# Kernel tuning notes

Measured on AMD Instinct MI355X. Metric: run time of the kernel, lower is better.

The kernel has to match this reference:

```python
import jax, jax.numpy as jnp
import numpy as np

B, S, D = 4, 2048, 1024
H, DK, DV = 16, 64, 64
FF = 4096
EPS = 1e-6


def _ln(x, g, b):
    mu = jnp.mean(x, axis=-1, keepdims=True)
    var = jnp.mean((x - mu) ** 2, axis=-1, keepdims=True)
    return (x - mu) * jax.lax.rsqrt(var + EPS) * g + b


def setup_inputs() -> dict:
    key = jax.random.key(0)
    ks = jax.random.split(key, 12)
    sd = 0.02
    return {
        "src": jax.random.normal(ks[0], (B, S, D), jnp.float32),
        "attn_mask": jnp.zeros((B, S, S), jnp.bool_),
        "Wq": jax.random.normal(ks[1], (D, H * DK), jnp.float32) * sd,
        "bq": jnp.zeros((H * DK,), jnp.float32),
        "Wk": jax.random.normal(ks[2], (D, H * DK), jnp.float32) * sd,
        "bk": jnp.zeros((H * DK,), jnp.float32),
        "Wv": jax.random.normal(ks[3], (D, H * DV), jnp.float32) * sd,
        "bv": jnp.zeros((H * DV,), jnp.float32),
        "Wo": jax.random.normal(ks[4], (D, D), jnp.float32) * sd,
        "bo": jnp.zeros((D,), jnp.float32),
        "ln1_g": jnp.ones((D,), jnp.float32),
        "ln1_b": jnp.zeros((D,), jnp.float32),
        "W1": jax.random.normal(ks[5], (D, FF), jnp.float32) * sd,
        "b1": jnp.zeros((FF,), jnp.float32),
        "W2": jax.random.normal(ks[6], (FF, D), jnp.float32) * sd,
        "b2": jnp.zeros((D,), jnp.float32),
        "ln2_g": jnp.ones((D,), jnp.float32),
        "ln2_b": jnp.zeros((D,), jnp.float32),
    }


def reference(src, attn_mask, Wq, bq, Wk, bk, Wv, bv, Wo, bo,
              ln1_g, ln1_b, W1, b1, W2, b2, ln2_g, ln2_b):
    # QKV projections, split heads: [B,S,H*dk] -> [B,H,S,dk]
    q = (src @ Wq + bq).reshape(B, S, H, DK).transpose(0, 2, 1, 3)
    k = (src @ Wk + bk).reshape(B, S, H, DK).transpose(0, 2, 1, 3)
    v = (src @ Wv + bv).reshape(B, S, H, DV).transpose(0, 2, 1, 3)

    scale = 1.0 / (DK ** 0.5)
    scores = jnp.einsum("bhqd,bhkd->bhqk", q, k) * scale
    scores = jnp.where(attn_mask[:, None, :, :], -1e9, scores)
    attn = jax.nn.softmax(scores, axis=-1)  # dropout = identity (eval)
    ctx = jnp.einsum("bhqk,bhkd->bhqd", attn, v)
    ctx = ctx.transpose(0, 2, 1, 3).reshape(B, S, D)

    att_out = ctx @ Wo + bo  # dropout = identity (eval)
    x = _ln(src + att_out, ln1_g, ln1_b)

    h = jax.nn.relu(x @ W1 + b1)  # dropout = identity (eval)
    ffn_out = h @ W2 + b2
    return _ln(ffn_out + x, ln2_g, ln2_b)
```

## Files before the change

kernel.cpp:

```cpp
#include <hip/hip_runtime.h>
#include <stdint.h>

#define BB 4
#define SS 2048
#define DMODEL 1024
#define NH 16
#define FF 4096
#define MROWS (BB*SS)

typedef __bf16 bf16x8 __attribute__((ext_vector_type(8)));
typedef __bf16 bf16x2t __attribute__((ext_vector_type(2)));
typedef float f32x4 __attribute__((ext_vector_type(4)));
typedef float f32x16 __attribute__((ext_vector_type(16)));
typedef unsigned uintx4 __attribute__((ext_vector_type(4)));

__device__ __forceinline__ unsigned short f2b(float f) {
  unsigned u = __float_as_uint(f);
  unsigned r = (u + 0x7FFFu + ((u >> 16) & 1u)) >> 16;
  return (unsigned short)r;
}
__device__ __forceinline__ float b2f(unsigned short u) {
  return __uint_as_float((unsigned)u << 16);
}

__device__ __forceinline__ unsigned pack2bf(float a, float b) {
  bf16x2t v = {(__bf16)a, (__bf16)b};
  return __builtin_bit_cast(unsigned, v);
}

__device__ __forceinline__ void pls32(unsigned& x, unsigned& y) {
#if defined(__has_builtin) && __has_builtin(__builtin_amdgcn_permlane32_swap)
  auto r = __builtin_amdgcn_permlane32_swap(x, y, 0, 0);
  x = (unsigned)r[0];
  y = (unsigned)r[1];
#else
  const unsigned sx = (unsigned)__shfl_xor((int)x, 32, 64);
  const unsigned sy = (unsigned)__shfl_xor((int)y, 32, 64);
  const bool hi = ((threadIdx.x >> 5) & 1) != 0;
  const unsigned nx = hi ? sy : x;
  const unsigned ny = hi ? y : sx;
  x = nx; y = ny;
#endif
}

__device__ __forceinline__ void gload_lds16(const void* g, void* l) {
  __builtin_amdgcn_global_load_lds(
      (const __attribute__((address_space(1))) void*)g,
      (__attribute__((address_space(3))) void*)l, 16, 0, 0);
}

__device__ __forceinline__ bf16x8 lds_frag(const unsigned short* base, int row, int k) {
  unsigned off = (unsigned)((row * 128 + k * 2) ^ ((row & 7) << 4));
  return *reinterpret_cast<const bf16x8*>(reinterpret_cast<const char*>(base) + off);
}

__device__ __forceinline__ bf16x8 frag_rot(const unsigned short* base, int row, int kElem) {
  const int cb = kElem * 2;
  const unsigned off = (unsigned)(row * 128 + ((((cb >> 4) + row) & 7) << 4) + (cb & 15));
  return *reinterpret_cast<const bf16x8*>(reinterpret_cast<const char*>(base) + off);
}

__global__ __launch_bounds__(256) void f32_to_bf16_k(const float* __restrict__ in,
                                                     unsigned short* __restrict__ out, int n8) {
  const int i = blockIdx.x * 256 + threadIdx.x;
  if (i >= n8) return;
  const float4* p = reinterpret_cast<const float4*>(in) + (size_t)i * 2;
  const float4 a = p[0], c = p[1];
  uint4 o;
  o.x = (unsigned)f2b(a.x) | ((unsigned)f2b(a.y) << 16);
  o.y = (unsigned)f2b(a.z) | ((unsigned)f2b(a.w) << 16);
  o.z = (unsigned)f2b(c.x) | ((unsigned)f2b(c.y) << 16);
  o.w = (unsigned)f2b(c.z) | ((unsigned)f2b(c.w) << 16);
  reinterpret_cast<uint4*>(out)[i] = o;
}

__global__ __launch_bounds__(256) void transpose_convert4_k(
    const float* __restrict__ i0, const float* __restrict__ i1,
    const float* __restrict__ i2, const float* __restrict__ i3,
    unsigned short* __restrict__ o0, unsigned short* __restrict__ o1,
    unsigned short* __restrict__ o2, unsigned short* __restrict__ o3) {
  __shared__ float tile[32][33];
  const int z = blockIdx.z;
  const float* in = (z == 0) ? i0 : (z == 1) ? i1 : (z == 2) ? i2 : i3;
  unsigned short* out = (z == 0) ? o0 : (z == 1) ? o1 : (z == 2) ? o2 : o3;
  const int c0 = blockIdx.x * 32, r0 = blockIdx.y * 32;
  const int tx = threadIdx.x, ty = threadIdx.y;
  #pragma unroll
  for (int i = 0; i < 4; ++i)
    tile[ty + i * 8][tx] = in[(size_t)(r0 + ty + i * 8) * 1024 + c0 + tx];
  __syncthreads();
  #pragma unroll
  for (int i = 0; i < 4; ++i)
    out[(size_t)(c0 + ty + i * 8) * 1024 + r0 + tx] = f2b(tile[tx][ty + i * 8]);
}

__global__ __launch_bounds__(256) void transpose_convert_k(const float* __restrict__ in,
                                                           unsigned short* __restrict__ out,
                                                           int R, int C) {
  __shared__ float tile[32][33];
  const int c0 = blockIdx.x * 32, r0 = blockIdx.y * 32;
  const int tx = threadIdx.x, ty = threadIdx.y;
  #pragma unroll
  for (int i = 0; i < 4; ++i)
    tile[ty + i * 8][tx] = in[(size_t)(r0 + ty + i * 8) * C + c0 + tx];
  __syncthreads();
  #pragma unroll
  for (int i = 0; i < 4; ++i)
    out[(size_t)(c0 + ty + i * 8) * R + r0 + tx] = f2b(tile[tx][ty + i * 8]);
}

__global__ __launch_bounds__(256) void v_transpose_k(const unsigned short* __restrict__ Vb,
                                                     unsigned short* __restrict__ Vt) {
  __shared__ unsigned short tile[32][33];
  const int bh = blockIdx.z, b = bh >> 4, h = bh & 15;
  const int s0 = blockIdx.x * 32, d0 = blockIdx.y * 32;
  const int tx = threadIdx.x, ty = threadIdx.y;
  #pragma unroll
  for (int i = 0; i < 4; ++i)
    tile[ty + i * 8][tx] = Vb[(size_t)(b * SS + s0 + ty + i * 8) * DMODEL + h * 64 + d0 + tx];
  __syncthreads();
  #pragma unroll
  for (int i = 0; i < 4; ++i)
    Vt[(size_t)(bh * 64 + d0 + ty + i * 8) * SS + s0 + tx] = tile[tx][ty + i * 8];
}

__global__ __launch_bounds__(256) void mask_pack_k(const unsigned char* __restrict__ mask,
                                                   unsigned long long* __restrict__ mbits, int total) {
  const int idx = blockIdx.x * 256 + threadIdx.x;
  if (idx >= total) return;
  const uint4* p = reinterpret_cast<const uint4*>(mask) + (size_t)idx * 4;
  unsigned long long bits = 0ull;
  #pragma unroll
  for (int q = 0; q < 4; ++q) {
    uint4 v = p[q];
    unsigned wds[4] = {v.x, v.y, v.z, v.w};
    #pragma unroll
    for (int j = 0; j < 4; ++j)
      #pragma unroll
      for (int by = 0; by < 4; ++by)
        if ((wds[j] >> (by * 8)) & 0xFFu) bits |= 1ull << (q * 16 + j * 4 + by);
  }
  mbits[idx] = bits;
}

#define CQ 0.18033688011112042f
template <int EPI>
__global__ __launch_bounds__(256, 3) void gemm2_k(const unsigned short* __restrict__ A,
                                                  const unsigned short* __restrict__ Bt,
                                                  const float* __restrict__ bias_a,
                                                  const float* __restrict__ bias_b,
                                                  const float* __restrict__ bias_c,
                                                  void* __restrict__ Cout, int N, int K) {
  __shared__ __align__(16) unsigned short As[2][128 * 64];
  __shared__ __align__(16) unsigned short Bs[2][128 * 64];
  const int t = threadIdx.x;
  const int lane = t & 63, w = t >> 6;
  const int wr = w >> 1, wc = w & 1;
  const int lr = lane & 15, lg = lane >> 4;

  const int nwg = gridDim.x;
  const int q8 = nwg >> 3;
  const int wg = (blockIdx.x & 7) * q8 + (blockIdx.x >> 3);
  const int sid = wg >> 6, within = wg & 63;
  const int smb = sid & 7, snb = sid >> 3;
  const int mb = smb * 8 + (within & 7);
  const int nb = snb * 8 + (within >> 3);
  const int m0 = mb * 128, n0 = nb * 128;

  const int srow = t >> 3;
  const unsigned cxor = (unsigned)(((t & 7) * 16) ^ (((t >> 3) & 7) << 4));
  const char* Asrc = reinterpret_cast<const char*>(A) + ((size_t)(m0 + srow) * K) * 2 + cxor;
  const char* Bsrc = reinterpret_cast<const char*>(Bt) + ((size_t)(n0 + srow) * K) * 2 + cxor;
  const size_t rstep = (size_t)32 * K * 2;
  char* AsB[2] = {reinterpret_cast<char*>(As[0]) + w * 1024, reinterpret_cast<char*>(As[1]) + w * 1024};
  char* BsB[2] = {reinterpret_cast<char*>(Bs[0]) + w * 1024, reinterpret_cast<char*>(Bs[1]) + w * 1024};

  auto stage = [&](int buf, int kt) {
    const char* ak = Asrc + (size_t)kt * 128;
    const char* bk = Bsrc + (size_t)kt * 128;
    #pragma unroll
    for (int c = 0; c < 4; ++c) {
      gload_lds16(ak + c * rstep, AsB[buf] + c * 4096);
      gload_lds16(bk + c * rstep, BsB[buf] + c * 4096);
    }
  };

  f32x4 acc[4][4] = {};
  const int nt = K >> 6;

  stage(0, 0);
  stage(1, 1);
  asm volatile("s_waitcnt vmcnt(8)" ::: "memory");
  __builtin_amdgcn_s_barrier();

  int cur = 0;
  for (int kt = 0; kt < nt; ++kt) {
    bf16x8 af[2][4], bfr[2][4];
    #pragma unroll
    for (int kk = 0; kk < 2; ++kk) {
      #pragma unroll
      for (int m = 0; m < 4; ++m)
        af[kk][m] = lds_frag(As[cur], wr * 64 + m * 16 + lr, kk * 32 + lg * 8);
      #pragma unroll
      for (int n = 0; n < 4; ++n)
        bfr[kk][n] = lds_frag(Bs[cur], wc * 64 + n * 16 + lr, kk * 32 + lg * 8);
    }
    __builtin_amdgcn_s_setprio(1);
    #pragma unroll
    for (int m = 0; m < 4; ++m)
      #pragma unroll
      for (int n = 0; n < 4; ++n)
        acc[m][n] = __builtin_amdgcn_mfma_f32_16x16x32_bf16(af[0][m], bfr[0][n], acc[m][n], 0, 0, 0);
    __builtin_amdgcn_s_setprio(0);

    asm volatile("s_waitcnt lgkmcnt(0)" ::: "memory");
    __builtin_amdgcn_s_barrier();
    if (kt + 2 < nt) {
      stage(cur, kt + 2);
      asm volatile("s_waitcnt vmcnt(8)" ::: "memory");
    } else {
      asm volatile("s_waitcnt vmcnt(0)" ::: "memory");
    }
    __builtin_amdgcn_s_barrier();

    __builtin_amdgcn_s_setprio(1);
    #pragma unroll
    for (int m = 0; m < 4; ++m)
      #pragma unroll
      for (int n = 0; n < 4; ++n)
        acc[m][n] = __builtin_amdgcn_mfma_f32_16x16x32_bf16(af[1][m], bfr[1][n], acc[m][n], 0, 0, 0);
    __builtin_amdgcn_s_setprio(0);
    cur ^= 1;
  }

  const int ccol0 = wc * 64;
  if constexpr (EPI == 3) {
    const int g3 = n0 >> 10;
    const float* bias = (g3 == 0) ? bias_a : (g3 == 1) ? bias_b : bias_c;
    const float scl = (g3 == 0) ? CQ : 1.0f;
    unsigned short* Og = reinterpret_cast<unsigned short*>(Cout) + (size_t)g3 * MROWS * DMODEL;
    const int ncol0 = (n0 & 1023) + ccol0;
    float bv[4];
    #pragma unroll
    for (int n = 0; n < 4; ++n) bv[n] = bias[ncol0 + n * 16 + lr];
    #pragma unroll
    for (int m = 0; m < 4; ++m)
      #pragma unroll
      for (int n = 0; n < 4; ++n)
        #pragma unroll
        for (int i = 0; i < 4; ++i) {
          const float v = (acc[m][n][i] + bv[n]) * scl;
          const size_t row = (size_t)(m0 + wr * 64 + m * 16 + lg * 4 + i);
          Og[row * DMODEL + (ncol0 + n * 16 + lr)] = f2b(v);
        }
  } else {
    float bv[4];
    #pragma unroll
    for (int n = 0; n < 4; ++n) bv[n] = bias_a[n0 + ccol0 + n * 16 + lr];
    #pragma unroll
    for (int m = 0; m < 4; ++m)
      #pragma unroll
      for (int n = 0; n < 4; ++n)
        #pragma unroll
        for (int i = 0; i < 4; ++i) {
          float v = acc[m][n][i] + bv[n];
          if (EPI == 1) v = fmaxf(v, 0.0f);
          const size_t row = (size_t)(m0 + wr * 64 + m * 16 + lg * 4 + i);
          const size_t col = (size_t)(n0 + ccol0 + n * 16 + lr);
          reinterpret_cast<unsigned short*>(Cout)[row * N + col] = f2b(v);
        }
  }
}

__global__ __launch_bounds__(256) void attn8_k(const unsigned short* __restrict__ Qb,
                                               const unsigned short* __restrict__ Kb,
                                               const unsigned short* __restrict__ Vt,
                                               const unsigned long long* __restrict__ mbits,
                                               unsigned short* __restrict__ ctx) {
  __shared__ __align__(16) unsigned short smem[16384];
  unsigned short* KsC = smem;
  unsigned short* KsN = smem + 4096;
  unsigned short* VsC = smem + 8192;
  unsigned short* VsN = smem + 12288;

  const int t = threadIdx.x;
  const int lane = t & 63, w = t >> 6;
  const int lo = lane & 31, hi = lane >> 5;

  const int flat = blockIdx.x;
  const int bid = (flat & 7) * 128 + (flat >> 3);
  const int bh = bid >> 4, qb = bid & 15;
  const int b = bh >> 4, h = bh & 15;
  const int q0 = qb * 128 + w * 32;

  bf16x8 qf[4];
  {
    const unsigned short* qp = Qb + (size_t)(b * SS + q0 + lo) * DMODEL + h * 64 + hi * 8;
    #pragma unroll
    for (int ds = 0; ds < 4; ++ds) qf[ds] = *reinterpret_cast<const bf16x8*>(qp + ds * 16);
  }

  const uintx4 onesw = {0x3F803F80u, 0x3F803F80u, 0x3F803F80u, 0x3F803F80u};
  const bf16x8 ones = __builtin_bit_cast(bf16x8, onesw);

  f32x16 ao0 = {}, ao1 = {}, dacc = {};

  const int srow = t >> 3;
  const int gsw = ((t & 7) - srow) & 7;
  const char* Ksrc = reinterpret_cast<const char*>(Kb) +
                     ((size_t)(b * SS + srow) * DMODEL + h * 64 + gsw * 8) * 2;
  const char* Vsrc = reinterpret_cast<const char*>(Vt) +
                     ((size_t)(bh * 64 + srow) * SS + gsw * 8) * 2;
  const unsigned wdo = (unsigned)(w * 1024);

  auto stage = [&](int kv, unsigned short* Kbuf, unsigned short* Vbuf) {
    const char* ks0 = Ksrc + (size_t)kv * (64 * DMODEL * 2);
    const char* vs0 = Vsrc + (size_t)kv * 128;
    char* kd = reinterpret_cast<char*>(Kbuf) + wdo;
    char* vd = reinterpret_cast<char*>(Vbuf) + wdo;
    gload_lds16(ks0, kd);
    gload_lds16(ks0 + (size_t)32 * DMODEL * 2, kd + 4096);
    gload_lds16(vs0, vd);
    gload_lds16(vs0 + (size_t)32 * SS * 2, vd + 4096);
  };

  const unsigned long long* mrow = mbits + (size_t)(b * SS + q0 + lo) * (SS / 64);

  stage(0, KsC, VsC);
  asm volatile("s_waitcnt vmcnt(0)" ::: "memory");
  __syncthreads();

  for (int kv = 0; kv < SS / 64; ++kv) {
    if (kv + 1 < SS / 64) stage(kv + 1, KsN, VsN);

    const unsigned long long mb = mrow[kv];

    f32x16 st0 = {}, st1 = {};
    __builtin_amdgcn_s_setprio(1);
    #pragma unroll
    for (int ds = 0; ds < 4; ++ds) {
      const int kcol = ds * 16 + hi * 8;
      const bf16x8 k0 = frag_rot(KsC, lo, kcol);
      const bf16x8 k1 = frag_rot(KsC, 32 + lo, kcol);
      st0 = __builtin_amdgcn_mfma_f32_32x32x16_bf16(k0, qf[ds], st0, 0, 0, 0);
      st1 = __builtin_amdgcn_mfma_f32_32x32x16_bf16(k1, qf[ds], st1, 0, 0, 0);
    }
    __builtin_amdgcn_s_setprio(0);

    if (__any(mb != 0ull)) {
      #pragma unroll
      for (int r = 0; r < 16; ++r) {
        const int k = (r & 3) + 8 * (r >> 2) + 4 * hi;
        if ((mb >> k) & 1ull) st0[r] = -20.0f;
        if ((mb >> (k + 32)) & 1ull) st1[r] = -20.0f;
      }
    }

    #pragma unroll
    for (int r = 0; r < 16; ++r) {
      st0[r] = exp2f(st0[r]);
      st1[r] = exp2f(st1[r]);
    }

    unsigned pw[16];
    #define PACK8(SV, KB)                                            \
      {                                                              \
        unsigned c0 = pack2bf(SV[0], SV[1]);                         \
        unsigned c1 = pack2bf(SV[2], SV[3]);                         \
        unsigned c2 = pack2bf(SV[4], SV[5]);                         \
        unsigned c3 = pack2bf(SV[6], SV[7]);                         \
        unsigned c4 = pack2bf(SV[8], SV[9]);                         \
        unsigned c5 = pack2bf(SV[10], SV[11]);                       \
        unsigned c6 = pack2bf(SV[12], SV[13]);                       \
        unsigned c7 = pack2bf(SV[14], SV[15]);                       \
        pls32(c0, c2); pls32(c1, c3); pls32(c4, c6); pls32(c5, c7);  \
        pw[(KB) + 0] = c0; pw[(KB) + 1] = c1;                        \
        pw[(KB) + 2] = c2; pw[(KB) + 3] = c3;                        \
        pw[(KB) + 4] = c4; pw[(KB) + 5] = c5;                        \
        pw[(KB) + 6] = c6; pw[(KB) + 7] = c7;                        \
      }
    PACK8(st0, 0)
    PACK8(st1, 8)
    #undef PACK8

    __builtin_amdgcn_s_setprio(1);
    #pragma unroll
    for (int ks = 0; ks < 4; ++ks) {
      const uintx4 pv = {pw[ks * 4 + 0], pw[ks * 4 + 1], pw[ks * 4 + 2], pw[ks * 4 + 3]};
      const bf16x8 pb = __builtin_bit_cast(bf16x8, pv);
      const int scol = ks * 16 + hi * 8;
      ao0 = __builtin_amdgcn_mfma_f32_32x32x16_bf16(frag_rot(VsC, lo, scol), pb, ao0, 0, 0, 0);
      ao1 = __builtin_amdgcn_mfma_f32_32x32x16_bf16(frag_rot(VsC, 32 + lo, scol), pb, ao1, 0, 0, 0);
      dacc = __builtin_amdgcn_mfma_f32_32x32x16_bf16(ones, pb, dacc, 0, 0, 0);
    }
    __builtin_amdgcn_s_setprio(0);

    asm volatile("s_waitcnt vmcnt(0)" ::: "memory");
    __syncthreads();
    unsigned short* tk = KsC; KsC = KsN; KsN = tk;
    unsigned short* tv = VsC; VsC = VsN; VsN = tv;
  }

  const float inv = 1.0f / dacc[0];
  unsigned short* Ob = smem + w * 2048;
  #pragma unroll
  for (int dt = 0; dt < 2; ++dt) {
    #pragma unroll
    for (int r = 0; r < 16; ++r) {
      const int d = dt * 32 + (r & 3) + 8 * (r >> 2) + 4 * hi;
      const float v = (dt ? ao1[r] : ao0[r]) * inv;
      const unsigned off = (unsigned)((lo * 128 + d * 2) ^ ((lo & 7) << 4));
      *reinterpret_cast<unsigned short*>(reinterpret_cast<char*>(Ob) + off) = f2b(v);
    }
  }
  __syncthreads();
  const int rr = lane >> 1, xh = (lane & 1) * 64;
  char* crow_g = reinterpret_cast<char*>(ctx) +
                 ((size_t)(b * SS + q0 + rr) * DMODEL + h * 64) * 2;
  #pragma unroll
  for (int c = 0; c < 4; ++c) {
    const unsigned off = (unsigned)((rr * 128 + xh + c * 16) ^ ((rr & 7) << 4));
    const uint4 vv = *reinterpret_cast<const uint4*>(reinterpret_cast<const char*>(Ob) + off);
    *reinterpret_cast<uint4*>(crow_g + xh + c * 16) = vv;
  }
}

__global__ __launch_bounds__(256) void ln1_k(const unsigned short* __restrict__ a,
                                             const float* __restrict__ res,
                                             const float* __restrict__ g,
                                             const float* __restrict__ be,
                                             unsigned short* __restrict__ ob) {
  const int row = blockIdx.x, t = threadIdx.x;
  const ushort4 av = reinterpret_cast<const ushort4*>(a + (size_t)row * DMODEL)[t];
  const float4 r = reinterpret_cast<const float4*>(res + (size_t)row * DMODEL)[t];
  float v0 = b2f(av.x) + r.x, v1 = b2f(av.y) + r.y;
  float v2 = b2f(av.z) + r.z, v3 = b2f(av.w) + r.w;
  float s = v0 + v1 + v2 + v3;
  float ss = v0 * v0 + v1 * v1 + v2 * v2 + v3 * v3;
  #pragma unroll
  for (int off = 1; off < 64; off <<= 1) {
    s += __shfl_xor(s, off, 64);
    ss += __shfl_xor(ss, off, 64);
  }
  __shared__ float red[8];
  const int wv = t >> 6;
  if ((t & 63) == 0) { red[wv] = s; red[4 + wv] = ss; }
  __syncthreads();
  s = red[0] + red[1] + red[2] + red[3];
  ss = red[4] + red[5] + red[6] + red[7];
  const float mu = s * (1.0f / DMODEL);
  const float rs = rsqrtf(ss * (1.0f / DMODEL) - mu * mu + 1e-6f);
  const float4 gg = reinterpret_cast<const float4*>(g)[t];
  const float4 bb = reinterpret_cast<const float4*>(be)[t];
  ushort4 u;
  u.x = f2b((v0 - mu) * rs * gg.x + bb.x);
  u.y = f2b((v1 - mu) * rs * gg.y + bb.y);
  u.z = f2b((v2 - mu) * rs * gg.z + bb.z);
  u.w = f2b((v3 - mu) * rs * gg.w + bb.w);
  reinterpret_cast<ushort4*>(ob + (size_t)row * DMODEL)[t] = u;
}

__global__ __launch_bounds__(256) void ln2_k(const unsigned short* __restrict__ a,
                                             const unsigned short* __restrict__ res,
                                             const float* __restrict__ g,
                                             const float* __restrict__ be,
                                             float* __restrict__ of) {
  const int row = blockIdx.x, t = threadIdx.x;
  const ushort4 av = reinterpret_cast<const ushort4*>(a + (size_t)row * DMODEL)[t];
  const ushort4 rv = reinterpret_cast<const ushort4*>(res + (size_t)row * DMODEL)[t];
  float v0 = b2f(av.x) + b2f(rv.x), v1 = b2f(av.y) + b2f(rv.y);
  float v2 = b2f(av.z) + b2f(rv.z), v3 = b2f(av.w) + b2f(rv.w);
  float s = v0 + v1 + v2 + v3;
  float ss = v0 * v0 + v1 * v1 + v2 * v2 + v3 * v3;
  #pragma unroll
  for (int off = 1; off < 64; off <<= 1) {
    s += __shfl_xor(s, off, 64);
    ss += __shfl_xor(ss, off, 64);
  }
  __shared__ float red[8];
  const int wv = t >> 6;
  if ((t & 63) == 0) { red[wv] = s; red[4 + wv] = ss; }
  __syncthreads();
  s = red[0] + red[1] + red[2] + red[3];
  ss = red[4] + red[5] + red[6] + red[7];
  const float mu = s * (1.0f / DMODEL);
  const float rs = rsqrtf(ss * (1.0f / DMODEL) - mu * mu + 1e-6f);
  const float4 gg = reinterpret_cast<const float4*>(g)[t];
  const float4 bb = reinterpret_cast<const float4*>(be)[t];
  float4 o;
  o.x = (v0 - mu) * rs * gg.x + bb.x;
  o.y = (v1 - mu) * rs * gg.y + bb.y;
  o.z = (v2 - mu) * rs * gg.z + bb.z;
  o.w = (v3 - mu) * rs * gg.w + bb.w;
  reinterpret_cast<float4*>(of + (size_t)row * DMODEL)[t] = o;
}

extern "C" void kernel_launch(void* const* d_in, const int* in_sizes, int n_in,
                              void* d_out, int out_size, void* d_ws, size_t ws_size,
                              hipStream_t stream) {
  const float* src = (const float*)d_in[0];
  const unsigned char* mask = (const unsigned char*)d_in[1];
  const float* Wq = (const float*)d_in[2];
  const float* bq = (const float*)d_in[3];
  const float* Wk = (const float*)d_in[4];
  const float* bk = (const float*)d_in[5];
  const float* Wv = (const float*)d_in[6];
  const float* bv = (const float*)d_in[7];
  const float* Wo = (const float*)d_in[8];
  const float* bo = (const float*)d_in[9];
  const float* ln1_g = (const float*)d_in[10];
  const float* ln1_b = (const float*)d_in[11];
  const float* W1 = (const float*)d_in[12];
  const float* b1 = (const float*)d_in[13];
  const float* W2 = (const float*)d_in[14];
  const float* b2 = (const float*)d_in[15];
  const float* ln2_g = (const float*)d_in[16];
  const float* ln2_b = (const float*)d_in[17];

  char* ws = (char*)d_ws;
  size_t off = 0;
  auto alloc = [&](size_t bytes) {
    char* p = ws + off;
    off += (bytes + 255) & ~(size_t)255;
    return p;
  };
  unsigned short* srcb = (unsigned short*)alloc((size_t)MROWS * DMODEL * 2);
  unsigned short* WqT  = (unsigned short*)alloc((size_t)DMODEL * DMODEL * 2);
  unsigned short* WkT  = (unsigned short*)alloc((size_t)DMODEL * DMODEL * 2);
  unsigned short* WvT  = (unsigned short*)alloc((size_t)DMODEL * DMODEL * 2);
  unsigned short* WoT  = (unsigned short*)alloc((size_t)DMODEL * DMODEL * 2);
  unsigned short* W1T  = (unsigned short*)alloc((size_t)FF * DMODEL * 2);
  unsigned short* W2T  = (unsigned short*)alloc((size_t)DMODEL * FF * 2);
  unsigned short* Qb   = (unsigned short*)alloc((size_t)MROWS * DMODEL * 2);
  unsigned short* Kb   = (unsigned short*)alloc((size_t)MROWS * DMODEL * 2);
  unsigned short* Vb   = (unsigned short*)alloc((size_t)MROWS * DMODEL * 2);
  unsigned short* Vt   = (unsigned short*)alloc((size_t)MROWS * DMODEL * 2);
  unsigned short* ctx  = (unsigned short*)alloc((size_t)MROWS * DMODEL * 2);
  unsigned short* aob  = (unsigned short*)alloc((size_t)MROWS * DMODEL * 2);
  unsigned short* xb   = (unsigned short*)alloc((size_t)MROWS * DMODEL * 2);
  unsigned short* fob  = (unsigned short*)alloc((size_t)MROWS * DMODEL * 2);
  unsigned short* hb   = (unsigned short*)alloc((size_t)MROWS * FF * 2);
  unsigned long long* mbits = (unsigned long long*)alloc((size_t)BB * SS * (SS / 64) * 8);
  float* outf = (float*)d_out;
  (void)Kb; (void)Vb;

  f32_to_bf16_k<<<(MROWS * DMODEL / 8 + 255) / 256, 256, 0, stream>>>(src, srcb, MROWS * DMODEL / 8);
  dim3 tb(32, 8);
  transpose_convert4_k<<<dim3(32, 32, 4), tb, 0, stream>>>(Wq, Wk, Wv, Wo, WqT, WkT, WvT, WoT);
  transpose_convert_k<<<dim3(FF / 32, 32), tb, 0, stream>>>(W1, W1T, DMODEL, FF);
  transpose_convert_k<<<dim3(32, FF / 32), tb, 0, stream>>>(W2, W2T, FF, DMODEL);
  mask_pack_k<<<(BB * SS * (SS / 64) + 255) / 256, 256, 0, stream>>>(mask, mbits, BB * SS * (SS / 64));

  gemm2_k<3><<<dim3(64 * 24), 256, 0, stream>>>(srcb, WqT, bq, bk, bv, Qb, 3072, DMODEL);

  v_transpose_k<<<dim3(SS / 32, 2, BB * NH), tb, 0, stream>>>(Vb, Vt);

  attn8_k<<<dim3((SS / 128) * BB * NH), 256, 0, stream>>>(Qb, Kb, Vt, mbits, ctx);

  gemm2_k<0><<<dim3(64 * 8), 256, 0, stream>>>(ctx, WoT, bo, nullptr, nullptr, aob, DMODEL, DMODEL);

  ln1_k<<<MROWS, 256, 0, stream>>>(aob, src, ln1_g, ln1_b, xb);

  gemm2_k<1><<<dim3(64 * 32), 256, 0, stream>>>(xb, W1T, b1, nullptr, nullptr, hb, FF, DMODEL);
  gemm2_k<0><<<dim3(64 * 8), 256, 0, stream>>>(hb, W2T, b2, nullptr, nullptr, fob, DMODEL, FF);

  ln2_k<<<MROWS, 256, 0, stream>>>(fob, xb, ln2_g, ln2_b, outf);
}
```

Before: 425.1 us.

## Split attention tile into halves, replace ones-MFMA row sum, read bf16 residual

The attention kernel now processes each 64-key tile in two 32-key halves, computing QK, exp, pack and PV per half. This cuts live registers, and launch bounds request 3 blocks per SM. The softmax denominator is now summed with VALU adds and a cross-half shuffle instead of an extra MFMA against a ones vector, which removes a third of the PV-phase MFMAs. The LN1 residual now reads the bf16 copy of src instead of fp32, halving that read traffic at the cost of some residual precision.

```diff
diff --git a/kernel.cpp b/kernel.cpp
--- a/kernel.cpp
+++ b/kernel.cpp
@@ -272,11 +272,11 @@
   }
 }
 
-__global__ __launch_bounds__(256) void attn8_k(const unsigned short* __restrict__ Qb,
-                                               const unsigned short* __restrict__ Kb,
-                                               const unsigned short* __restrict__ Vt,
-                                               const unsigned long long* __restrict__ mbits,
-                                               unsigned short* __restrict__ ctx) {
+__global__ __launch_bounds__(256, 3) void attn9_k(const unsigned short* __restrict__ Qb,
+                                                  const unsigned short* __restrict__ Kb,
+                                                  const unsigned short* __restrict__ Vt,
+                                                  const unsigned long long* __restrict__ mbits,
+                                                  unsigned short* __restrict__ ctx) {
   __shared__ __align__(16) unsigned short smem[16384];
   unsigned short* KsC = smem;
   unsigned short* KsN = smem + 4096;
@@ -300,10 +300,8 @@
     for (int ds = 0; ds < 4; ++ds) qf[ds] = *reinterpret_cast<const bf16x8*>(qp + ds * 16);
   }
 
-  const uintx4 onesw = {0x3F803F80u, 0x3F803F80u, 0x3F803F80u, 0x3F803F80u};
-  const bf16x8 ones = __builtin_bit_cast(bf16x8, onesw);
-
-  f32x16 ao0 = {}, ao1 = {}, dacc = {};
+  f32x16 ao0 = {}, ao1 = {};
+  float lsum = 0.0f;
 
   const int srow = t >> 3;
   const int gsw = ((t & 7) - srow) & 7;
@@ -334,66 +332,65 @@
     if (kv + 1 < SS / 64) stage(kv + 1, KsN, VsN);
 
     const unsigned long long mb = mrow[kv];
-
-    f32x16 st0 = {}, st1 = {};
-    __builtin_amdgcn_s_setprio(1);
-    #pragma unroll
-    for (int ds = 0; ds < 4; ++ds) {
-      const int kcol = ds * 16 + hi * 8;
-      const bf16x8 k0 = frag_rot(KsC, lo, kcol);
-      const bf16x8 k1 = frag_rot(KsC, 32 + lo, kcol);
-      st0 = __builtin_amdgcn_mfma_f32_32x32x16_bf16(k0, qf[ds], st0, 0, 0, 0);
-      st1 = __builtin_amdgcn_mfma_f32_32x32x16_bf16(k1, qf[ds], st1, 0, 0, 0);
+    float ls = 0.0f;
+
+    #pragma unroll
+    for (int half = 0; half < 2; ++half) {
+      f32x16 st = {};
+      __builtin_amdgcn_s_setprio(1);
+      #pragma unroll
+      for (int ds = 0; ds < 4; ++ds) {
+        const int kcol = ds * 16 + hi * 8;
+        st = __builtin_amdgcn_mfma_f32_32x32x16_bf16(
+            frag_rot(KsC, half * 32 + lo, kcol), qf[ds], st, 0, 0, 0);
+      }
+      __builtin_amdgcn_s_setprio(0);
+
+      if (__any(mb != 0ull)) {
+        #pragma unroll
+        for (int r = 0; r < 16; ++r) {
+          const int k = (r & 3) + 8 * (r >> 2) + 4 * hi + 32 * half;
+          if ((mb >> k) & 1ull) st[r] = -20.0f;
+        }
+      }
+
+      #pragma unroll
+      for (int r = 0; r < 16; ++r) st[r] = exp2f(st[r]);
+      {
+        float ps[8];
+        #pragma unroll
+        for (int r = 0; r < 8; ++r) ps[r] = st[r] + st[r + 8];
+        #pragma unroll
+        for (int r = 0; r < 4; ++r) ps[r] += ps[r + 4];
+        ls += (ps[0] + ps[1]) + (ps[2] + ps[3]);
+      }
+
+      unsigned c0 = pack2bf(st[0], st[1]);
+      unsigned c1 = pack2bf(st[2], st[3]);
+      unsigned c2 = pack2bf(st[4], st[5]);
+      unsigned c3 = pack2bf(st[6], st[7]);
+      unsigned c4 = pack2bf(st[8], st[9]);
+      unsigned c5 = pack2bf(st[10], st[11]);
+      unsigned c6 = pack2bf(st[12], st[13]);
+      unsigned c7 = pack2bf(st[14], st[15]);
+      pls32(c0, c2); pls32(c1, c3); pls32(c4, c6); pls32(c5, c7);
+
+      const uintx4 pv0 = {c0, c1, c2, c3};
+      const uintx4 pv1 = {c4, c5, c6, c7};
+      const bf16x8 pb0 = __builtin_bit_cast(bf16x8, pv0);
+      const bf16x8 pb1 = __builtin_bit_cast(bf16x8, pv1);
+      const int s0c = (half * 2 + 0) * 16 + hi * 8;
+      const int s1c = (half * 2 + 1) * 16 + hi * 8;
+      __builtin_amdgcn_s_setprio(1);
+      ao0 = __builtin_amdgcn_mfma_f32_32x32x16_bf16(frag_rot(VsC, lo, s0c), pb0, ao0, 0, 0, 0);
+      ao1 = __builtin_amdgcn_mfma_f32_32x32x16_bf16(frag_rot(VsC, 32 + lo, s0c), pb0, ao1, 0, 0, 0);
+      ao0 = __builtin_amdgcn_mfma_f32_32x32x16_bf16(frag_rot(VsC, lo, s1c), pb1, ao0, 0, 0, 0);
+      ao1 = __builtin_amdgcn_mfma_f32_32x32x16_bf16(frag_rot(VsC, 32 + lo, s1c), pb1, ao1, 0, 0, 0);
+      __builtin_amdgcn_s_setprio(0);
     }
-    __builtin_amdgcn_s_setprio(0);
-
-    if (__any(mb != 0ull)) {
-      #pragma unroll
-      for (int r = 0; r < 16; ++r) {
-        const int k = (r & 3) + 8 * (r >> 2) + 4 * hi;
-        if ((mb >> k) & 1ull) st0[r] = -20.0f;
-        if ((mb >> (k + 32)) & 1ull) st1[r] = -20.0f;
-      }
-    }
-
-    #pragma unroll
-    for (int r = 0; r < 16; ++r) {
-      st0[r] = exp2f(st0[r]);
-      st1[r] = exp2f(st1[r]);
-    }
-
-    unsigned pw[16];
-    #define PACK8(SV, KB)                                            \
-      {                                                              \
-        unsigned c0 = pack2bf(SV[0], SV[1]);                         \
-        unsigned c1 = pack2bf(SV[2], SV[3]);                         \
-        unsigned c2 = pack2bf(SV[4], SV[5]);                         \
-        unsigned c3 = pack2bf(SV[6], SV[7]);                         \
-        unsigned c4 = pack2bf(SV[8], SV[9]);                         \
-        unsigned c5 = pack2bf(SV[10], SV[11]);                       \
-        unsigned c6 = pack2bf(SV[12], SV[13]);                       \
-        unsigned c7 = pack2bf(SV[14], SV[15]);                       \
-        pls32(c0, c2); pls32(c1, c3); pls32(c4, c6); pls32(c5, c7);  \
-        pw[(KB) + 0] = c0; pw[(KB) + 1] = c1;                        \
-        pw[(KB) + 2] = c2; pw[(KB) + 3] = c3;                        \
-        pw[(KB) + 4] = c4; pw[(KB) + 5] = c5;                        \
-        pw[(KB) + 6] = c6; pw[(KB) + 7] = c7;                        \
-      }
-    PACK8(st0, 0)
-    PACK8(st1, 8)
-    #undef PACK8
-
-    __builtin_amdgcn_s_setprio(1);
-    #pragma unroll
-    for (int ks = 0; ks < 4; ++ks) {
-      const uintx4 pv = {pw[ks * 4 + 0], pw[ks * 4 + 1], pw[ks * 4 + 2], pw[ks * 4 + 3]};
-      const bf16x8 pb = __builtin_bit_cast(bf16x8, pv);
-      const int scol = ks * 16 + hi * 8;
-      ao0 = __builtin_amdgcn_mfma_f32_32x32x16_bf16(frag_rot(VsC, lo, scol), pb, ao0, 0, 0, 0);
-      ao1 = __builtin_amdgcn_mfma_f32_32x32x16_bf16(frag_rot(VsC, 32 + lo, scol), pb, ao1, 0, 0, 0);
-      dacc = __builtin_amdgcn_mfma_f32_32x32x16_bf16(ones, pb, dacc, 0, 0, 0);
-    }
-    __builtin_amdgcn_s_setprio(0);
+
+    ls += __shfl_xor(ls, 32, 64);
+    lsum += ls;
 
     asm volatile("s_waitcnt vmcnt(0)" ::: "memory");
     __syncthreads();
@@ -401,7 +398,7 @@
     unsigned short* tv = VsC; VsC = VsN; VsN = tv;
   }
 
-  const float inv = 1.0f / dacc[0];
+  const float inv = 1.0f / lsum;
   unsigned short* Ob = smem + w * 2048;
   #pragma unroll
   for (int dt = 0; dt < 2; ++dt) {
@@ -426,15 +423,15 @@
 }
 
 __global__ __launch_bounds__(256) void ln1_k(const unsigned short* __restrict__ a,
-                                             const float* __restrict__ res,
+                                             const unsigned short* __restrict__ res,
                                              const float* __restrict__ g,
                                              const float* __restrict__ be,
                                              unsigned short* __restrict__ ob) {
   const int row = blockIdx.x, t = threadIdx.x;
   const ushort4 av = reinterpret_cast<const ushort4*>(a + (size_t)row * DMODEL)[t];
-  const float4 r = reinterpret_cast<const float4*>(res + (size_t)row * DMODEL)[t];
-  float v0 = b2f(av.x) + r.x, v1 = b2f(av.y) + r.y;
-  float v2 = b2f(av.z) + r.z, v3 = b2f(av.w) + r.w;
+  const ushort4 rv = reinterpret_cast<const ushort4*>(res + (size_t)row * DMODEL)[t];
+  float v0 = b2f(av.x) + b2f(rv.x), v1 = b2f(av.y) + b2f(rv.y);
+  float v2 = b2f(av.z) + b2f(rv.z), v3 = b2f(av.w) + b2f(rv.w);
   float s = v0 + v1 + v2 + v3;
   float ss = v0 * v0 + v1 * v1 + v2 * v2 + v3 * v3;
   #pragma unroll
@@ -555,11 +552,11 @@
 
   v_transpose_k<<<dim3(SS / 32, 2, BB * NH), tb, 0, stream>>>(Vb, Vt);
 
-  attn8_k<<<dim3((SS / 128) * BB * NH), 256, 0, stream>>>(Qb, Kb, Vt, mbits, ctx);
+  attn9_k<<<dim3((SS / 128) * BB * NH), 256, 0, stream>>>(Qb, Kb, Vt, mbits, ctx);
 
   gemm2_k<0><<<dim3(64 * 8), 256, 0, stream>>>(ctx, WoT, bo, nullptr, nullptr, aob, DMODEL, DMODEL);
 
-  ln1_k<<<MROWS, 256, 0, stream>>>(aob, src, ln1_g, ln1_b, xb);
+  ln1_k<<<MROWS, 256, 0, stream>>>(aob, srcb, ln1_g, ln1_b, xb);
 
   gemm2_k<1><<<dim3(64 * 32), 256, 0, stream>>>(xb, W1T, b1, nullptr, nullptr, hb, FF, DMODEL);
   gemm2_k<0><<<dim3(64 * 8), 256, 0, stream>>>(hb, W2T, b2, nullptr, nullptr, fob, DMODEL, FF);
```

After: 415.6 us (median of 2 runs). 2.2% less time.
